# Optimization experiments

Measured on AMD Instinct MI355X. Metric: run time of the kernel, lower is better.

Reference implementation:

```python
import jax, jax.numpy as jnp
import numpy as np

N, D, H, K = 50000, 384, 128, 16
WALK_STEPS = 3
EPS = 1e-8


def setup_inputs() -> dict:
    key = jax.random.key(0)
    ks = jax.random.split(key, 7)
    emb = jax.random.normal(ks[0], (N, D), dtype=jnp.float32)
    qv = jax.random.normal(ks[1], (D,), dtype=jnp.float32)
    W1 = jax.random.normal(ks[2], (2 * D, H), dtype=jnp.float32) * (1.0 / np.sqrt(2 * D))
    b1 = jax.random.normal(ks[3], (H,), dtype=jnp.float32) * 0.01
    W2 = jax.random.normal(ks[4], (H, K), dtype=jnp.float32) * (1.0 / np.sqrt(H))
    b2 = jax.random.normal(ks[5], (K,), dtype=jnp.float32) * 0.01
    nbr = jax.random.randint(ks[6], (N, K), 0, N, dtype=jnp.int64)
    return {"emb": emb, "qv": qv, "W1": W1, "b1": b1, "W2": W2, "b2": b2, "nbr": nbr}


def reference(emb, qv, W1, b1, W2, b2, nbr):
    n, k = nbr.shape
    # Per-node coin: coin_net(concat(emb_i, qv)) -> normalized rank-1 outer product.
    # (Coin does not depend on the walk state, so compute once; original recomputes
    # the identical values every step.)
    inp = jnp.concatenate([emb, jnp.broadcast_to(qv, (n, qv.shape[0]))], axis=-1)  # [n, 2d]
    h = jax.nn.relu(inp @ W1 + b1)                                                 # [n, H]
    amps = h @ W2 + b2                                                             # [n, k]
    amps = amps / (jnp.linalg.norm(amps, axis=-1, keepdims=True) + EPS)
    coin = amps[:, :, None] * amps[:, None, :]                                     # [n, k, k]
    fro = jnp.linalg.norm(coin.reshape(n, -1), axis=-1)[:, None, None]
    coin = coin / (fro + EPS)
    # Reverse-slot lookup: for edge slot (i, idx) with j = nbr[i, idx], find first p
    # with nbr[j, p] == i (the .index(i) in the original); missing -> dropped.
    match = nbr[nbr] == jnp.arange(n, dtype=nbr.dtype)[:, None, None]              # [n, k, k]
    rev_idx = jnp.argmax(match, axis=-1)                                           # [n, k]
    rev_mask = jnp.any(match, axis=-1)                                             # [n, k]
    flat_tgt = (nbr * k + rev_idx).reshape(-1)
    # Initial state is real and the coin is real (cast to cfloat in the original),
    # so the walk state stays real-valued; |z|^2 == z^2 here.
    state = jnp.full((n, k), 1.0 / np.sqrt(n * k), dtype=emb.dtype)

    def step(state, _):
        s_p = jnp.einsum('nij,nj->ni', coin, state)                                # coin @ state
        contrib = jnp.where(rev_mask, s_p, 0.0)
        new = jnp.zeros(n * k, dtype=state.dtype).at[flat_tgt].add(contrib.reshape(-1))
        new = new.reshape(n, k)
        new = new / (jnp.sqrt(jnp.sum(new * new)) + EPS)
        return new, None

    state, _ = jax.lax.scan(step, state, None, length=WALK_STEPS)
    probs = jnp.sum(state * state, axis=1)
    return jnp.nan_to_num(probs, nan=0.0, posinf=1.0, neginf=0.0)
```

## Files before the change

### kernel.cpp

```cpp
#include <hip/hip_runtime.h>
#include <hip/hip_bf16.h>
#include <math.h>

#define N_NODES 50000
#define DIM     384
#define HID     128
#define KN      16
#define NK      (N_NODES * KN)
#define EPSF    1e-8f
#define CAPR    2048
#define CAPN    2048

#define OFF_CNT    0u
#define OFF_C1     256u
#define OFF_RSRC   1024u
#define OFF_RTGT   9216u
#define OFF_NLIST  17408u
#define OFF_INVF   25600u
#define OFF_SUMA   33792u
#define OFF_AC     41984u
#define OFF_MAP    173056u
#define OFF_SLOT   373056u

#define RECIP_BLOCKS ((NK + 511) / 512)

__global__ __launch_bounds__(512)
void init_kernel(int* __restrict__ nodemap, float* __restrict__ out,
                 int* __restrict__ counters) {
    int i = blockIdx.x * 512 + threadIdx.x;
    if (i < N_NODES) { nodemap[i] = -1; out[i] = 0.0f; }
    if (i == 0) { counters[0] = 0; counters[1] = 0; }
}

__global__ __launch_bounds__(512)
void recip_c1_kernel(const int* __restrict__ nbr,
                     const float* __restrict__ qv,
                     const float* __restrict__ W1,
                     const float* __restrict__ b1,
                     float* __restrict__ c1,
                     int* __restrict__ counters,
                     int* __restrict__ rec_src,
                     int* __restrict__ rec_tgt,
                     int* __restrict__ slotmap,
                     int* __restrict__ nodemap,
                     int* __restrict__ nodelist) {
    if (blockIdx.x == RECIP_BLOCKS) {
        __shared__ float sq[DIM];
        __shared__ float part[4][HID];
        int t = threadIdx.x;
        if (t < DIM) sq[t] = qv[t];
        __syncthreads();
        int c = t & 127, g = t >> 7;
        const float* wp = W1 + (size_t)(DIM + g * 96) * HID + c;
        float acc = 0.f;
        #pragma unroll 8
        for (int d = 0; d < 96; ++d)
            acc += sq[g * 96 + d] * wp[(size_t)d * HID];
        part[g][c] = acc;
        __syncthreads();
        if (t < HID)
            c1[t] = b1[t] + part[0][t] + part[1][t] + part[2][t] + part[3][t];
        return;
    }
    int e = blockIdx.x * 512 + threadIdx.x;
    if (e >= NK) return;
    int i = e >> 4;
    int j = nbr[e];
    const int* row = nbr + (size_t)j * KN;
    int p = -1;
    #pragma unroll
    for (int q = KN - 1; q >= 0; --q)
        if (row[q] == i) p = q;
    if (p < 0) return;
    int r = atomicAdd(&counters[0], 1);
    if (r < CAPR) {
        rec_src[r] = e;
        rec_tgt[r] = j * KN + p;
        slotmap[e] = r;
    }
    int old = atomicCAS(&nodemap[i], -1, -2);
    if (old == -1) {
        int ni = atomicAdd(&counters[1], 1);
        if (ni < CAPN) { nodelist[ni] = i; nodemap[i] = ni; }
        else           { nodemap[i] = 0; }
    }
}

__global__ __launch_bounds__(512)
void coin_kernel(const float* __restrict__ emb,
                 const float* __restrict__ W1,
                 const float* __restrict__ W2,
                 const float* __restrict__ b2,
                 const float* __restrict__ c1,
                 const int* __restrict__ counters,
                 const int* __restrict__ nodelist,
                 float* __restrict__ a_c,
                 float* __restrict__ invf_c,
                 float* __restrict__ suma_c) {
    int nn = counters[1]; if (nn > CAPN) nn = CAPN;
    int b = blockIdx.x;
    if (b >= nn) return;
    int node = nodelist[b];

    __shared__ float se[DIM];
    __shared__ float part[4][HID];
    __shared__ float sh[HID];
    __shared__ float part2[32][KN];
    __shared__ float samps[KN];

    int t = threadIdx.x;
    if (t < DIM) se[t] = emb[(size_t)node * DIM + t];
    __syncthreads();

    int c = t & 127, g = t >> 7;
    const float* wp = W1 + (size_t)(g * 96) * HID + c;
    float acc = 0.f;
    #pragma unroll 8
    for (int d = 0; d < 96; ++d)
        acc += se[g * 96 + d] * wp[(size_t)d * HID];
    part[g][c] = acc;
    __syncthreads();
    if (t < HID)
        sh[t] = fmaxf(c1[t] + part[0][t] + part[1][t] + part[2][t] + part[3][t], 0.f);
    __syncthreads();

    int k = t & 15, g2 = t >> 4;
    float a2 = 0.f;
    #pragma unroll
    for (int jj = 0; jj < 4; ++jj)
        a2 += sh[g2 * 4 + jj] * W2[(size_t)(g2 * 4 + jj) * KN + k];
    part2[g2][k] = a2;
    __syncthreads();
    if (t < KN) {
        float s = b2[t];
        #pragma unroll
        for (int g3 = 0; g3 < 32; ++g3) s += part2[g3][t];
        samps[t] = s;
    }
    __syncthreads();

    if (t == 0) {
        float ss = 0.f;
        #pragma unroll
        for (int q = 0; q < KN; ++q) ss += samps[q] * samps[q];
        float inv_na = 1.0f / (sqrtf(ss) + EPSF);
        float fro = 0.f, sa = 0.f;
        #pragma unroll
        for (int q = 0; q < KN; ++q) {
            float av = samps[q] * inv_na;
            a_c[b * KN + q] = av;
            fro += av * av;
            sa  += av;
        }
        invf_c[b] = 1.0f / (fro + EPSF);
        suma_c[b] = sa;
    }
}

#define NORM_LDS(buf)                                                      \
    {                                                                      \
        float part = 0.f;                                                  \
        for (int r = tid; r < M; r += 512) part += buf[r] * buf[r];        \
        red[tid] = part; __syncthreads();                                  \
        for (int off = 256; off > 0; off >>= 1) {                          \
            if (tid < off) red[tid] += red[tid + off];                     \
            __syncthreads();                                               \
        }                                                                  \
        if (tid == 0) s_inv = 1.0f / (sqrtf(red[0]) + EPSF);               \
        __syncthreads();                                                   \
        for (int r = tid; r < M; r += 512) buf[r] *= s_inv;                \
        __syncthreads();                                                   \
    }

__global__ __launch_bounds__(512)
void walk_kernel(const int* __restrict__ counters,
                 const int* __restrict__ rec_src,
                 const int* __restrict__ rec_tgt,
                 const int* __restrict__ slotmap,
                 const int* __restrict__ nodemap,
                 const int* __restrict__ nodelist,
                 const float* __restrict__ a_c,
                 const float* __restrict__ invf_c,
                 const float* __restrict__ suma_c,
                 float* __restrict__ out) {
    __shared__ int   trecL[CAPR];
    __shared__ int   ciL[CAPR];
    __shared__ float asL[CAPR];
    __shared__ float faL[CAPR];
    __shared__ float stA[CAPR];
    __shared__ float stB[CAPR];
    __shared__ float dotL[CAPN];
    __shared__ float red[512];
    __shared__ float s_inv;

    int tid = threadIdx.x;
    int M  = counters[0]; if (M  > CAPR) M  = CAPR;
    int NN = counters[1]; if (NN > CAPN) NN = CAPN;
    const float S0 = 1.0f / sqrtf((float)N_NODES * (float)KN);

    for (int r = tid; r < M; r += 512) {
        int s  = rec_src[r];
        trecL[r] = slotmap[rec_tgt[r]];
        int ci = nodemap[s >> 4];
        ciL[r] = ci;
        float av = a_c[ci * KN + (s & 15)];
        asL[r] = av;
        faL[r] = av * invf_c[ci];
        stA[r] = 0.f;
        stB[r] = 0.f;
    }
    for (int ci = tid; ci < NN; ci += 512)
        dotL[ci] = S0 * suma_c[ci];
    __syncthreads();

    for (int r = tid; r < M; r += 512)
        atomicAdd(&stA[trecL[r]], faL[r] * dotL[ciL[r]]);
    __syncthreads();
    NORM_LDS(stA)

    for (int ci = tid; ci < NN; ci += 512) dotL[ci] = 0.f;
    __syncthreads();
    for (int r = tid; r < M; r += 512)
        atomicAdd(&dotL[ciL[r]], asL[r] * stA[r]);
    __syncthreads();
    for (int r = tid; r < M; r += 512)
        atomicAdd(&stB[trecL[r]], faL[r] * dotL[ciL[r]]);
    __syncthreads();
    NORM_LDS(stB)

    for (int ci = tid; ci < NN; ci += 512) dotL[ci] = 0.f;
    __syncthreads();
    for (int r = tid; r < M; r += 512)
        atomicAdd(&dotL[ciL[r]], asL[r] * stB[r]);
    __syncthreads();
    for (int r = tid; r < M; r += 512) stA[r] = 0.f;
    __syncthreads();
    for (int r = tid; r < M; r += 512)
        atomicAdd(&stA[trecL[r]], faL[r] * dotL[ciL[r]]);
    __syncthreads();
    NORM_LDS(stA)

    for (int r = tid; r < M; r += 512) {
        float v = stA[r];
        atomicAdd(&out[nodelist[ciL[r]]], v * v);
    }
}

extern "C" void kernel_launch(void* const* d_in, const int* in_sizes, int n_in,
                              void* d_out, int out_size, void* d_ws, size_t ws_size,
                              hipStream_t stream) {
    const float* emb = (const float*)d_in[0];
    const float* qv  = (const float*)d_in[1];
    const float* W1  = (const float*)d_in[2];
    const float* b1  = (const float*)d_in[3];
    const float* W2  = (const float*)d_in[4];
    const float* b2  = (const float*)d_in[5];
    const int*   nbr = (const int*)d_in[6];
    float*       out = (float*)d_out;

    char* ws = (char*)d_ws;
    int*   counters = (int*)(ws + OFF_CNT);
    float* c1       = (float*)(ws + OFF_C1);
    int*   rec_src  = (int*)(ws + OFF_RSRC);
    int*   rec_tgt  = (int*)(ws + OFF_RTGT);
    int*   nodelist = (int*)(ws + OFF_NLIST);
    float* invf_c   = (float*)(ws + OFF_INVF);
    float* suma_c   = (float*)(ws + OFF_SUMA);
    float* a_c      = (float*)(ws + OFF_AC);
    int*   nodemap  = (int*)(ws + OFF_MAP);
    int*   slotmap  = (int*)(ws + OFF_SLOT);

    init_kernel<<<(N_NODES + 511) / 512, 512, 0, stream>>>(nodemap, out, counters);
    recip_c1_kernel<<<RECIP_BLOCKS + 1, 512, 0, stream>>>(
        nbr, qv, W1, b1, c1, counters, rec_src, rec_tgt, slotmap, nodemap, nodelist);
    coin_kernel<<<CAPN, 512, 0, stream>>>(
        emb, W1, W2, b2, c1, counters, nodelist, a_c, invf_c, suma_c);
    walk_kernel<<<1, 512, 0, stream>>>(
        counters, rec_src, rec_tgt, slotmap, nodemap, nodelist,
        a_c, invf_c, suma_c, out);
}
```

Before: 34.34 us.

## Fuse reciprocal scan, coin MLP and walk into one persistent kernel with grid barriers

Merges the init and c1 kernels into one launch, and folds the reciprocal-edge scan, per-node coin MLP and the single-block walk into one persistent 256-block kernel separated by software grid barriers. This removes two kernel launches and their inter-kernel gaps. The walk's LDS tree reduction is replaced by a wavefront shuffle reduction. The cost is spin-wait barriers that depend on all 256 blocks being co-resident, plus grid-stride loops that give less parallelism than the original per-item launches.

```diff
diff --git a/kernel.cpp b/kernel.cpp
--- a/kernel.cpp
+++ b/kernel.cpp
@@ -1,5 +1,4 @@
 #include <hip/hip_runtime.h>
-#include <hip/hip_bf16.h>
 #include <math.h>
 
 #define N_NODES 50000
@@ -10,190 +9,179 @@
 #define EPSF    1e-8f
 #define CAPR    2048
 #define CAPN    2048
+#define NBLK    256
 
 #define OFF_CNT    0u
-#define OFF_C1     256u
-#define OFF_RSRC   1024u
-#define OFF_RTGT   9216u
-#define OFF_NLIST  17408u
-#define OFF_INVF   25600u
-#define OFF_SUMA   33792u
-#define OFF_AC     41984u
-#define OFF_MAP    173056u
-#define OFF_SLOT   373056u
-
-#define RECIP_BLOCKS ((NK + 511) / 512)
+#define OFF_BARC   64u
+#define OFF_BARG   512u
+#define OFF_C1     1024u
+#define OFF_RSRC   2048u
+#define OFF_RTGT   10240u
+#define OFF_NLIST  18432u
+#define OFF_INVF   26624u
+#define OFF_SUMA   34816u
+#define OFF_AC     43008u
+#define OFF_MAP    174080u
+#define OFF_SLOT   374080u
+
+#define SMEM_BYTES ((6 * CAPR + CAPN + 16) * 4)
+
+__device__ __forceinline__ void grid_barrier(int* cnt, int* go) {
+    __syncthreads();
+    if (threadIdx.x == 0) {
+        __threadfence();
+        if (atomicAdd(cnt, 1) == NBLK - 1) {
+            __hip_atomic_store(go, 1, __ATOMIC_RELEASE, __HIP_MEMORY_SCOPE_AGENT);
+        } else {
+            while (__hip_atomic_load(go, __ATOMIC_ACQUIRE, __HIP_MEMORY_SCOPE_AGENT) == 0)
+                __builtin_amdgcn_s_sleep(2);
+        }
+        __threadfence();
+    }
+    __syncthreads();
+}
 
 __global__ __launch_bounds__(512)
-void init_kernel(int* __restrict__ nodemap, float* __restrict__ out,
-                 int* __restrict__ counters) {
-    int i = blockIdx.x * 512 + threadIdx.x;
-    if (i < N_NODES) { nodemap[i] = -1; out[i] = 0.0f; }
-    if (i == 0) { counters[0] = 0; counters[1] = 0; }
-}
-
-__global__ __launch_bounds__(512)
-void recip_c1_kernel(const int* __restrict__ nbr,
-                     const float* __restrict__ qv,
-                     const float* __restrict__ W1,
-                     const float* __restrict__ b1,
-                     float* __restrict__ c1,
-                     int* __restrict__ counters,
-                     int* __restrict__ rec_src,
-                     int* __restrict__ rec_tgt,
-                     int* __restrict__ slotmap,
-                     int* __restrict__ nodemap,
-                     int* __restrict__ nodelist) {
-    if (blockIdx.x == RECIP_BLOCKS) {
-        __shared__ float sq[DIM];
-        __shared__ float part[4][HID];
-        int t = threadIdx.x;
-        if (t < DIM) sq[t] = qv[t];
-        __syncthreads();
-        int c = t & 127, g = t >> 7;
-        const float* wp = W1 + (size_t)(DIM + g * 96) * HID + c;
-        float acc = 0.f;
-        #pragma unroll 8
-        for (int d = 0; d < 96; ++d)
-            acc += sq[g * 96 + d] * wp[(size_t)d * HID];
-        part[g][c] = acc;
-        __syncthreads();
-        if (t < HID)
-            c1[t] = b1[t] + part[0][t] + part[1][t] + part[2][t] + part[3][t];
+void init_c1_kernel(const float* __restrict__ qv,
+                    const float* __restrict__ W1,
+                    const float* __restrict__ b1,
+                    float* __restrict__ c1,
+                    int* __restrict__ counters,
+                    int* __restrict__ barc,
+                    int* __restrict__ barg,
+                    int* __restrict__ nodemap,
+                    float* __restrict__ out) {
+    int b = blockIdx.x, t = threadIdx.x;
+    if (b < 98) {
+        int i = b * 512 + t;
+        if (i < N_NODES) { nodemap[i] = -1; out[i] = 0.0f; }
         return;
     }
-    int e = blockIdx.x * 512 + threadIdx.x;
-    if (e >= NK) return;
-    int i = e >> 4;
-    int j = nbr[e];
-    const int* row = nbr + (size_t)j * KN;
-    int p = -1;
-    #pragma unroll
-    for (int q = KN - 1; q >= 0; --q)
-        if (row[q] == i) p = q;
-    if (p < 0) return;
-    int r = atomicAdd(&counters[0], 1);
-    if (r < CAPR) {
-        rec_src[r] = e;
-        rec_tgt[r] = j * KN + p;
-        slotmap[e] = r;
-    }
-    int old = atomicCAS(&nodemap[i], -1, -2);
-    if (old == -1) {
-        int ni = atomicAdd(&counters[1], 1);
-        if (ni < CAPN) { nodelist[ni] = i; nodemap[i] = ni; }
-        else           { nodemap[i] = 0; }
-    }
-}
-
-__global__ __launch_bounds__(512)
-void coin_kernel(const float* __restrict__ emb,
-                 const float* __restrict__ W1,
-                 const float* __restrict__ W2,
-                 const float* __restrict__ b2,
-                 const float* __restrict__ c1,
-                 const int* __restrict__ counters,
-                 const int* __restrict__ nodelist,
-                 float* __restrict__ a_c,
-                 float* __restrict__ invf_c,
-                 float* __restrict__ suma_c) {
-    int nn = counters[1]; if (nn > CAPN) nn = CAPN;
-    int b = blockIdx.x;
-    if (b >= nn) return;
-    int node = nodelist[b];
-
-    __shared__ float se[DIM];
-    __shared__ float part[4][HID];
-    __shared__ float sh[HID];
-    __shared__ float part2[32][KN];
-    __shared__ float samps[KN];
-
-    int t = threadIdx.x;
-    if (t < DIM) se[t] = emb[(size_t)node * DIM + t];
-    __syncthreads();
-
+    if (t < 4) { barc[t] = 0; barg[t] = 0; }
+    if (t < 2) counters[t] = 0;
+
+    __shared__ float sq[DIM];
+    __shared__ float part[4 * HID];
+    if (t < DIM) sq[t] = qv[t];
+    __syncthreads();
     int c = t & 127, g = t >> 7;
-    const float* wp = W1 + (size_t)(g * 96) * HID + c;
+    const float* wp = W1 + (size_t)(DIM + g * 96) * HID + c;
     float acc = 0.f;
     #pragma unroll 8
     for (int d = 0; d < 96; ++d)
-        acc += se[g * 96 + d] * wp[(size_t)d * HID];
-    part[g][c] = acc;
+        acc += sq[g * 96 + d] * wp[(size_t)d * HID];
+    part[g * HID + c] = acc;
     __syncthreads();
     if (t < HID)
-        sh[t] = fmaxf(c1[t] + part[0][t] + part[1][t] + part[2][t] + part[3][t], 0.f);
-    __syncthreads();
-
-    int k = t & 15, g2 = t >> 4;
-    float a2 = 0.f;
-    #pragma unroll
-    for (int jj = 0; jj < 4; ++jj)
-        a2 += sh[g2 * 4 + jj] * W2[(size_t)(g2 * 4 + jj) * KN + k];
-    part2[g2][k] = a2;
-    __syncthreads();
-    if (t < KN) {
-        float s = b2[t];
+        c1[t] = b1[t] + part[t] + part[HID + t] + part[2 * HID + t] + part[3 * HID + t];
+}
+
+__global__ __launch_bounds__(512)
+void fused_kernel(const float* __restrict__ emb,
+                  const float* __restrict__ W1,
+                  const float* __restrict__ W2,
+                  const float* __restrict__ b2,
+                  const int*   __restrict__ nbr,
+                  const float* __restrict__ c1,
+                  int* counters, int* barc, int* barg,
+                  int* rec_src, int* rec_tgt, int* slotmap,
+                  int* nodemap, int* nodelist,
+                  float* a_c, float* invf_c, float* suma_c,
+                  float* out) {
+    extern __shared__ char smem[];
+    int tid = threadIdx.x, bid = blockIdx.x;
+
+    for (int e = bid * 512 + tid; e < NK; e += NBLK * 512) {
+        int i = e >> 4;
+        int j = nbr[e];
+        const int* row = nbr + (size_t)j * KN;
+        int p = -1;
         #pragma unroll
-        for (int g3 = 0; g3 < 32; ++g3) s += part2[g3][t];
-        samps[t] = s;
-    }
-    __syncthreads();
-
-    if (t == 0) {
-        float ss = 0.f;
-        #pragma unroll
-        for (int q = 0; q < KN; ++q) ss += samps[q] * samps[q];
-        float inv_na = 1.0f / (sqrtf(ss) + EPSF);
-        float fro = 0.f, sa = 0.f;
-        #pragma unroll
-        for (int q = 0; q < KN; ++q) {
-            float av = samps[q] * inv_na;
-            a_c[b * KN + q] = av;
-            fro += av * av;
-            sa  += av;
-        }
-        invf_c[b] = 1.0f / (fro + EPSF);
-        suma_c[b] = sa;
-    }
-}
-
-#define NORM_LDS(buf)                                                      \
-    {                                                                      \
-        float part = 0.f;                                                  \
-        for (int r = tid; r < M; r += 512) part += buf[r] * buf[r];        \
-        red[tid] = part; __syncthreads();                                  \
-        for (int off = 256; off > 0; off >>= 1) {                          \
-            if (tid < off) red[tid] += red[tid + off];                     \
-            __syncthreads();                                               \
-        }                                                                  \
-        if (tid == 0) s_inv = 1.0f / (sqrtf(red[0]) + EPSF);               \
-        __syncthreads();                                                   \
-        for (int r = tid; r < M; r += 512) buf[r] *= s_inv;                \
-        __syncthreads();                                                   \
-    }
-
-__global__ __launch_bounds__(512)
-void walk_kernel(const int* __restrict__ counters,
-                 const int* __restrict__ rec_src,
-                 const int* __restrict__ rec_tgt,
-                 const int* __restrict__ slotmap,
-                 const int* __restrict__ nodemap,
-                 const int* __restrict__ nodelist,
-                 const float* __restrict__ a_c,
-                 const float* __restrict__ invf_c,
-                 const float* __restrict__ suma_c,
-                 float* __restrict__ out) {
-    __shared__ int   trecL[CAPR];
-    __shared__ int   ciL[CAPR];
-    __shared__ float asL[CAPR];
-    __shared__ float faL[CAPR];
-    __shared__ float stA[CAPR];
-    __shared__ float stB[CAPR];
-    __shared__ float dotL[CAPN];
-    __shared__ float red[512];
-    __shared__ float s_inv;
-
-    int tid = threadIdx.x;
+        for (int q = KN - 1; q >= 0; --q)
+            if (row[q] == i) p = q;
+        if (p < 0) continue;
+        int r = atomicAdd(&counters[0], 1);
+        if (r < CAPR) { rec_src[r] = e; rec_tgt[r] = j * KN + p; slotmap[e] = r; }
+        int old = atomicCAS(&nodemap[i], -1, -2);
+        if (old == -1) {
+            int ni = atomicAdd(&counters[1], 1);
+            if (ni < CAPN) { nodelist[ni] = i; nodemap[i] = ni; }
+            else           { nodemap[i] = 0; }
+        }
+    }
+    grid_barrier(&barc[0], &barg[0]);
+
+    {
+        float* se    = (float*)smem;
+        float* part  = se + 384;
+        float* sh    = part + 512;
+        float* part2 = sh + 128;
+        float* samps = part2 + 512;
+        int nn = __hip_atomic_load(&counters[1], __ATOMIC_RELAXED, __HIP_MEMORY_SCOPE_AGENT);
+        if (nn > CAPN) nn = CAPN;
+        for (int b = bid; b < nn; b += NBLK) {
+            int node = nodelist[b];
+            __syncthreads();
+            if (tid < DIM) se[tid] = emb[(size_t)node * DIM + tid];
+            __syncthreads();
+            int c = tid & 127, g = tid >> 7;
+            const float* wp = W1 + (size_t)(g * 96) * HID + c;
+            float acc = 0.f;
+            #pragma unroll 8
+            for (int d = 0; d < 96; ++d)
+                acc += se[g * 96 + d] * wp[(size_t)d * HID];
+            part[g * HID + c] = acc;
+            __syncthreads();
+            if (tid < HID)
+                sh[tid] = fmaxf(c1[tid] + part[tid] + part[HID + tid]
+                                + part[2 * HID + tid] + part[3 * HID + tid], 0.f);
+            __syncthreads();
+            int k = tid & 15, g2 = tid >> 4;
+            float a2 = 0.f;
+            #pragma unroll
+            for (int jj = 0; jj < 4; ++jj)
+                a2 += sh[g2 * 4 + jj] * W2[(size_t)(g2 * 4 + jj) * KN + k];
+            part2[g2 * KN + k] = a2;
+            __syncthreads();
+            if (tid < KN) {
+                float s = b2[tid];
+                #pragma unroll
+                for (int g3 = 0; g3 < 32; ++g3) s += part2[g3 * KN + tid];
+                samps[tid] = s;
+            }
+            __syncthreads();
+            if (tid == 0) {
+                float ss = 0.f;
+                #pragma unroll
+                for (int q = 0; q < KN; ++q) ss += samps[q] * samps[q];
+                float inv_na = 1.0f / (sqrtf(ss) + EPSF);
+                float fro = 0.f, sa = 0.f;
+                #pragma unroll
+                for (int q = 0; q < KN; ++q) {
+                    float av = samps[q] * inv_na;
+                    a_c[b * KN + q] = av;
+                    fro += av * av;
+                    sa  += av;
+                }
+                invf_c[b] = 1.0f / (fro + EPSF);
+                suma_c[b] = sa;
+            }
+        }
+    }
+    grid_barrier(&barc[1], &barg[1]);
+
+    if (bid != 0) return;
+
+    int*   trecL = (int*)smem;
+    int*   ciL   = trecL + CAPR;
+    float* asL   = (float*)(ciL + CAPR);
+    float* faL   = asL + CAPR;
+    float* stA   = faL + CAPR;
+    float* stB   = stA + CAPR;
+    float* dotL  = stB + CAPR;
+    float* red   = dotL + CAPN;
+    float* sinvp = red + 8;
+
     int M  = counters[0]; if (M  > CAPR) M  = CAPR;
     int NN = counters[1]; if (NN > CAPN) NN = CAPN;
     const float S0 = 1.0f / sqrtf((float)N_NODES * (float)KN);
@@ -213,10 +201,29 @@
         dotL[ci] = S0 * suma_c[ci];
     __syncthreads();
 
+    auto NORM = [&](float* buf) {
+        float part = 0.f;
+        for (int r = tid; r < M; r += 512) part += buf[r] * buf[r];
+        #pragma unroll
+        for (int off = 32; off > 0; off >>= 1) part += __shfl_xor(part, off, 64);
+        if ((tid & 63) == 0) red[tid >> 6] = part;
+        __syncthreads();
+        if (tid < 64) {
+            float v = (tid < 8) ? red[tid] : 0.f;
+            #pragma unroll
+            for (int off = 4; off > 0; off >>= 1) v += __shfl_xor(v, off, 64);
+            if (tid == 0) *sinvp = 1.0f / (sqrtf(v) + EPSF);
+        }
+        __syncthreads();
+        float si = *sinvp;
+        for (int r = tid; r < M; r += 512) buf[r] *= si;
+        __syncthreads();
+    };
+
     for (int r = tid; r < M; r += 512)
         atomicAdd(&stA[trecL[r]], faL[r] * dotL[ciL[r]]);
     __syncthreads();
-    NORM_LDS(stA)
+    NORM(stA);
 
     for (int ci = tid; ci < NN; ci += 512) dotL[ci] = 0.f;
     __syncthreads();
@@ -226,7 +233,7 @@
     for (int r = tid; r < M; r += 512)
         atomicAdd(&stB[trecL[r]], faL[r] * dotL[ciL[r]]);
     __syncthreads();
-    NORM_LDS(stB)
+    NORM(stB);
 
     for (int ci = tid; ci < NN; ci += 512) dotL[ci] = 0.f;
     __syncthreads();
@@ -238,7 +245,7 @@
     for (int r = tid; r < M; r += 512)
         atomicAdd(&stA[trecL[r]], faL[r] * dotL[ciL[r]]);
     __syncthreads();
-    NORM_LDS(stA)
+    NORM(stA);
 
     for (int r = tid; r < M; r += 512) {
         float v = stA[r];
@@ -260,6 +267,8 @@
 
     char* ws = (char*)d_ws;
     int*   counters = (int*)(ws + OFF_CNT);
+    int*   barc     = (int*)(ws + OFF_BARC);
+    int*   barg     = (int*)(ws + OFF_BARG);
     float* c1       = (float*)(ws + OFF_C1);
     int*   rec_src  = (int*)(ws + OFF_RSRC);
     int*   rec_tgt  = (int*)(ws + OFF_RTGT);
@@ -270,12 +279,10 @@
     int*   nodemap  = (int*)(ws + OFF_MAP);
     int*   slotmap  = (int*)(ws + OFF_SLOT);
 
-    init_kernel<<<(N_NODES + 511) / 512, 512, 0, stream>>>(nodemap, out, counters);
-    recip_c1_kernel<<<RECIP_BLOCKS + 1, 512, 0, stream>>>(
-        nbr, qv, W1, b1, c1, counters, rec_src, rec_tgt, slotmap, nodemap, nodelist);
-    coin_kernel<<<CAPN, 512, 0, stream>>>(
-        emb, W1, W2, b2, c1, counters, nodelist, a_c, invf_c, suma_c);
-    walk_kernel<<<1, 512, 0, stream>>>(
-        counters, rec_src, rec_tgt, slotmap, nodemap, nodelist,
+    init_c1_kernel<<<99, 512, 0, stream>>>(qv, W1, b1, c1, counters, barc, barg,
+                                           nodemap, out);
+    fused_kernel<<<NBLK, 512, SMEM_BYTES, stream>>>(
+        emb, W1, W2, b2, nbr, c1, counters, barc, barg,
+        rec_src, rec_tgt, slotmap, nodemap, nodelist,
         a_c, invf_c, suma_c, out);
 }
```

After: 94.47 us. 175% more time.
